# Kernel optimization log

Hardware: AMD Instinct MI355X
Metric: run time of the kernel (lower is better)

The kernel has to match this reference:

```python
import jax, jax.numpy as jnp
import numpy as np

B, S, H = 2, 256, 512
EPS = 1e-12  # TPLinker conditional LayerNorm default epsilon
NEG = -1e30  # finite stand-in for -inf in running max


def _cond_layer_norm(x, cond, Wg, Wb, gamma, beta):
    # TPLinker conditional LayerNorm: gamma/beta are modulated by a linear map of cond.
    g = gamma + cond @ Wg          # (..., H)
    b = beta + cond @ Wb           # (..., H)
    xc = x - jnp.mean(x, axis=-1, keepdims=True)
    inv = jax.lax.rsqrt(jnp.mean(xc * xc, axis=-1, keepdims=True) + EPS)
    return xc * inv * g + b


def setup_inputs() -> dict:
    key = jax.random.key(0)
    ks = jax.random.split(key, 6)
    return {
        "seq_hiddens": jax.random.normal(ks[0], (B, S, H), jnp.float32),
        "mask": jnp.ones((B, S), jnp.float32),
        "lamtha": jax.random.uniform(ks[1], (H,), jnp.float32),
        "Wg1": jax.random.normal(ks[2], (H, H), jnp.float32) * 0.02,
        "Wb1": jax.random.normal(ks[3], (H, H), jnp.float32) * 0.02,
        "g1": jnp.ones((H,), jnp.float32),
        "b1": jnp.zeros((H,), jnp.float32),
        "Wg2": jax.random.normal(ks[4], (H, H), jnp.float32) * 0.02,
        "Wb2": jax.random.normal(ks[5], (H, H), jnp.float32) * 0.02,
        "g2": jnp.ones((H,), jnp.float32),
        "b2": jnp.zeros((H,), jnp.float32),
    }


def reference(seq_hiddens, mask, lamtha, Wg1, Wb1, g1, b1, Wg2, Wb2, g2, b2):
    # mask additive penalty, broadcast over hidden (matches (1-mask)*-1000 expand)
    seq = seq_hiddens + ((1.0 - mask) * -1000.0)[:, :, None]  # (B,S,H)

    ii, jj = jnp.triu_indices(S)  # row-major pairs (i, j>=i), same order as the torch loop

    # window means over seq[i..j] via cumulative sums (replaces O(S^3) recomputation)
    csum = jnp.cumsum(seq, axis=1)                              # (B,S,H)
    lens = (jj - ii + 1).astype(seq.dtype)[None, :, None]
    mean_pairs = (csum[:, jj] - csum[:, ii] + seq[:, ii]) / lens  # (B,P,H)

    # window maxes over seq[i..j]: scan over j keeping running max per start i
    idx = jnp.arange(S)

    def step(state, j):
        sj = jnp.take(seq, j, axis=1)  # (B,H)
        new = jnp.where((idx <= j)[None, :, None],
                        jnp.maximum(state, sj[:, None, :]),
                        jnp.asarray(NEG, seq.dtype))
        return new, new

    _, Mall = jax.lax.scan(step, jnp.full((B, S, H), NEG, seq.dtype), idx)  # (S_j,B,S_i,H)
    max_pairs = Mall[jj, :, ii].transpose(1, 0, 2)  # (B,P,H)

    # mix pooling
    inner = lamtha * mean_pairs + (1.0 - lamtha) * max_pairs  # (B,P,H)

    visible = seq[:, jj]  # (B,P,H) token j
    repeat = seq[:, ii]   # (B,P,H) token i

    shaking = _cond_layer_norm(visible, repeat, Wg1, Wb1, g1, b1)
    return _cond_layer_norm(shaking, inner, Wg2, Wb2, g2, b2)
```

## Files before the change

kernel.cpp:

```cpp
#include <hip/hip_runtime.h>
#include <hip/hip_bf16.h>

typedef __hip_bfloat16 bf16;
typedef short short8 __attribute__((ext_vector_type(8)));
typedef float floatx4 __attribute__((ext_vector_type(4)));

#define S 256
#define H 512
#define P 32896
#define NROWS 65792
#define NEGF -1e30f
#define EPSF 1e-12f

#define OFF_SEQ    0u
#define OFF_CSUM   1048576u
#define OFF_LN1    2129920u
#define OFF_G1     3178496u
#define OFF_B1     4227072u
#define OFF_WCAT   5275648u
#define OFF_II     6324224u
#define OFF_JJ     6390016u
#define OFF_MU2    6455808u
#define OFF_INV2   6718976u
#define OFF_INNER  6982144u

__device__ __forceinline__ void gld_lds16(const void* g, void* l) {
    __builtin_amdgcn_global_load_lds(
        (const __attribute__((address_space(1))) void*)g,
        (__attribute__((address_space(3))) void*)l, 16, 0, 0);
}

__global__ __launch_bounds__(512) void prep_kernel(const float* __restrict__ Wg2,
                                                   const float* __restrict__ Wb2,
                                                   bf16* __restrict__ wcatT,
                                                   unsigned short* __restrict__ ii,
                                                   unsigned short* __restrict__ jj) {
    if (blockIdx.x < 1024) {
        int n = blockIdx.x, k = threadIdx.x;
        int tt = n >> 7, c = n & 127;
        int h = tt * 64 + (c & 63);
        float v = (c < 64) ? Wg2[(size_t)k * H + h] : Wb2[(size_t)k * H + h];
        wcatT[(size_t)n * H + k] = __float2bfloat16(v);
    } else {
        int p = (blockIdx.x - 1024) * 512 + threadIdx.x;
        if (p >= P) return;
        float disc = 513.0f * 513.0f - 8.0f * (float)p;
        int i = (int)((513.0f - sqrtf(disc)) * 0.5f);
        i = i < 0 ? 0 : (i > S - 1 ? S - 1 : i);
        while (i > 0 && (i * S - i * (i - 1) / 2) > p) --i;
        while (i < S - 1 && ((i + 1) * S - (i + 1) * i / 2) <= p) ++i;
        int off = i * S - i * (i - 1) / 2;
        ii[p] = (unsigned short)i;
        jj[p] = (unsigned short)(i + (p - off));
    }
}

__global__ __launch_bounds__(512) void seq_scan1_ln1(const float* __restrict__ x,
                                                     const float* __restrict__ mask,
                                                     float* __restrict__ seq, float* __restrict__ tot,
                                                     float* __restrict__ ln1) {
    __shared__ float part[8][8][2];
    __shared__ float rstat[8][2];
    int b = blockIdx.x >> 5, sc = blockIdx.x & 31, h = threadIdx.x;
    int wave = h >> 6, lane = h & 63;
    int s0 = sc * 8;
    float v[8];
    float run = 0.0f;
#pragma unroll
    for (int t = 0; t < 8; ++t) {
        int s = s0 + t;
        v[t] = x[(size_t)(b * S + s) * H + h] + (1.0f - mask[b * S + s]) * (-1000.0f);
        seq[(size_t)(b * S + s) * H + h] = v[t];
        run += v[t];
    }
    tot[(size_t)blockIdx.x * H + h] = run;
#pragma unroll
    for (int t = 0; t < 8; ++t) {
        float s = v[t], q = v[t] * v[t];
        for (int o = 1; o < 64; o <<= 1) { s += __shfl_xor(s, o); q += __shfl_xor(q, o); }
        if (lane == 0) { part[wave][t][0] = s; part[wave][t][1] = q; }
    }
    __syncthreads();
    if (h < 16) {
        int row = h >> 1, st = h & 1;
        float a = 0.0f;
#pragma unroll
        for (int w = 0; w < 8; ++w) a += part[w][row][st];
        rstat[row][st] = a;
    }
    __syncthreads();
#pragma unroll
    for (int t = 0; t < 8; ++t) {
        float m = rstat[t][0] * (1.0f / 512.0f);
        float var = rstat[t][1] * (1.0f / 512.0f) - m * m;
        var = var < 0.0f ? 0.0f : var;
        float inv = rsqrtf(var + EPSF);
        ln1[(size_t)(b * S + s0 + t) * H + h] = (v[t] - m) * inv;
    }
}

__global__ __launch_bounds__(512) void seq_scan2(const float* __restrict__ seq,
                                                 const float* __restrict__ tot,
                                                 float* __restrict__ csum) {
    int b = blockIdx.x >> 5, sc = blockIdx.x & 31, h = threadIdx.x;
    float run = 0.0f;
    for (int c = 0; c < sc; ++c) run += tot[(size_t)(b * 32 + c) * H + h];
    int s0 = sc * 8;
#pragma unroll
    for (int t = 0; t < 8; ++t) {
        run += seq[(size_t)(b * S + s0 + t) * H + h];
        csum[(size_t)(b * S + s0 + t) * H + h] = run;
    }
}

__global__ __launch_bounds__(512) void g1b1_kernel(
    const float* __restrict__ seq, const float* __restrict__ Wg1, const float* __restrict__ Wb1,
    const float* __restrict__ g1, const float* __restrict__ b1,
    float* __restrict__ G1, float* __restrict__ B1) {
    __shared__ float rowbuf[4][H];
    int grp = blockIdx.x;
    int mat = blockIdx.y;
    int h = threadIdx.x;
    int r0 = grp * 4;
    for (int r = 0; r < 4; ++r) rowbuf[r][h] = seq[(size_t)(r0 + r) * H + h];
    __syncthreads();
    const float* W = mat ? Wb1 : Wg1;
    float acc[4] = {0, 0, 0, 0};
#pragma unroll 8
    for (int k = 0; k < H; ++k) {
        float w = W[(size_t)k * H + h];
#pragma unroll
        for (int r = 0; r < 4; ++r) acc[r] += rowbuf[r][k] * w;
    }
    float bias = (mat ? b1 : g1)[h];
    float* dst = mat ? B1 : G1;
    for (int r = 0; r < 4; ++r) dst[(size_t)(r0 + r) * H + h] = acc[r] + bias;
}

__global__ __launch_bounds__(256) void inner_kernel(
    const float* __restrict__ seq, const float* __restrict__ csum,
    const float* __restrict__ lamtha, bf16* __restrict__ inner) {
    int id = blockIdx.x;
    int t = id & 255, b = id >> 8;
    int i = b ? (255 - t) : t;
    int h2 = threadIdx.x;
    float2 lam = ((const float2*)lamtha)[h2];
    float2 oml = {1.0f - lam.x, 1.0f - lam.y};
    const float2* seqb = (const float2*)(seq + (size_t)b * S * H);
    const float2* csb = (const float2*)(csum + (size_t)b * S * H);
    float2 s_i = seqb[i * 256 + h2];
    float2 c_i = csb[i * 256 + h2];
    float2 mrun = {NEGF, NEGF};
    size_t base = (size_t)b * P + (size_t)(i * S - i * (i - 1) / 2);
    __hip_bfloat162* dst = (__hip_bfloat162*)inner;
    int j = i;
#define INNER_STEP(vv, cc, jx)                                             \
    {                                                                      \
        mrun.x = fmaxf(mrun.x, vv.x);                                      \
        mrun.y = fmaxf(mrun.y, vv.y);                                      \
        float rl = 1.0f / (float)((jx) - i + 1);                           \
        float mx = (cc.x - c_i.x + s_i.x) * rl;                            \
        float my = (cc.y - c_i.y + s_i.y) * rl;                            \
        __hip_bfloat162 o;                                                 \
        o.x = __float2bfloat16(lam.x * mx + oml.x * mrun.x);               \
        o.y = __float2bfloat16(lam.y * my + oml.y * mrun.y);               \
        dst[(base + (size_t)((jx) - i)) * 256 + h2] = o;                   \
    }
    for (; j + 4 <= S; j += 4) {
        float2 v0 = seqb[(j + 0) * 256 + h2], c0 = csb[(j + 0) * 256 + h2];
        float2 v1 = seqb[(j + 1) * 256 + h2], c1 = csb[(j + 1) * 256 + h2];
        float2 v2 = seqb[(j + 2) * 256 + h2], c2 = csb[(j + 2) * 256 + h2];
        float2 v3 = seqb[(j + 3) * 256 + h2], c3 = csb[(j + 3) * 256 + h2];
        INNER_STEP(v0, c0, j + 0)
        INNER_STEP(v1, c1, j + 1)
        INNER_STEP(v2, c2, j + 2)
        INNER_STEP(v3, c3, j + 3)
    }
    for (; j < S; ++j) {
        float2 v = seqb[j * 256 + h2];
        float2 c = csb[j * 256 + h2];
        INNER_STEP(v, c, j)
    }
#undef INNER_STEP
}

__global__ void stats_kernel(const float* __restrict__ ln1, const float* __restrict__ G1,
                             const float* __restrict__ B1,
                             const unsigned short* __restrict__ ii,
                             const unsigned short* __restrict__ jj,
                             float* __restrict__ mu2, float* __restrict__ inv2) {
    int r = blockIdx.x * 4 + (threadIdx.x >> 6);
    int lane = threadIdx.x & 63;
    int b = (r >= P) ? 1 : 0;
    int p = r - b * P;
    int i = ii[p], j = jj[p];
    const float4* lp = (const float4*)(ln1 + (size_t)(b * S + j) * H);
    const float4* gp = (const float4*)(G1 + (size_t)(b * S + i) * H);
    const float4* bp = (const float4*)(B1 + (size_t)(b * S + i) * H);
    float sum = 0.0f, ss = 0.0f;
#pragma unroll
    for (int t = 0; t < 2; ++t) {
        int idx = t * 64 + lane;
        float4 a = lp[idx], g = gp[idx], bb = bp[idx];
        float v0 = a.x * g.x + bb.x, v1 = a.y * g.y + bb.y;
        float v2 = a.z * g.z + bb.z, v3 = a.w * g.w + bb.w;
        sum += (v0 + v1) + (v2 + v3);
        ss += (v0 * v0 + v1 * v1) + (v2 * v2 + v3 * v3);
    }
    for (int o = 1; o < 64; o <<= 1) { sum += __shfl_xor(sum, o); ss += __shfl_xor(ss, o); }
    if (lane == 0) {
        float m = sum * (1.0f / 512.0f);
        float var = ss * (1.0f / 512.0f) - m * m;
        var = var < 0.0f ? 0.0f : var;
        mu2[r] = m;
        inv2[r] = rsqrtf(var + EPSF);
    }
}

__global__ __launch_bounds__(256, 2) void gemm_kernel(
    const bf16* __restrict__ inner, const bf16* __restrict__ wcatT,
    const float* __restrict__ g2, const float* __restrict__ b2,
    const float* __restrict__ ln1, const float* __restrict__ G1, const float* __restrict__ B1,
    const unsigned short* __restrict__ ii, const unsigned short* __restrict__ jj,
    const float* __restrict__ mu2, const float* __restrict__ inv2,
    float* __restrict__ out) {
    extern __shared__ __align__(16) char smem[];

    const int tid = threadIdx.x;
    const int wave = tid >> 6, lane = tid & 63;
    const int q = lane >> 4, l15 = lane & 15;
    const int wm = wave & 1, wn = wave >> 1;

    const int id = blockIdx.x;
    int rb, t;
    if (id < 4096) { rb = (id >> 6) * 8 + (id & 7); t = (id >> 3) & 7; }
    else           { int w = id - 4096; rb = 512 + (w & 1); t = w >> 1; }
    const int R0 = rb * 128;

    const int srow = tid >> 3;
    const int sx8 = ((tid & 7) ^ (srow & 7)) * 8;
    const bf16* const Ag = inner + (size_t)(R0 + srow) * H + sx8;
    const bf16* const Bg = wcatT + (size_t)(t * 128 + srow) * H + sx8;

    char* const A0 = smem;
    char* const B0 = smem + 16384;
    char* const A1 = smem + 32768;
    char* const B1s = smem + 49152;

    floatx4 acc[4][4];
#pragma unroll
    for (int a = 0; a < 4; ++a)
#pragma unroll
        for (int c = 0; c < 4; ++c) acc[a][c] = (floatx4){0.f, 0.f, 0.f, 0.f};

    auto STAGE = [&](int kt, char* Ad, char* Bd) {
#pragma unroll
        for (int i2 = 0; i2 < 4; ++i2)
            gld_lds16(Ag + (size_t)i2 * 32 * H + kt * 64, Ad + i2 * 4096 + wave * 1024);
#pragma unroll
        for (int i2 = 0; i2 < 4; ++i2)
            gld_lds16(Bg + (size_t)i2 * 32 * H + kt * 64, Bd + i2 * 4096 + wave * 1024);
    };

    STAGE(0, A0, B0);
    STAGE(1, A1, B1s);
    asm volatile("s_waitcnt vmcnt(8)" ::: "memory");
    asm volatile("s_barrier" ::: "memory");

#pragma unroll
    for (int kt = 0; kt < 8; ++kt) {
        char* const As = (kt & 1) ? A1 : A0;
        char* const Bs = (kt & 1) ? B1s : B0;

        short8 bfr[4][2], af[4][2];
#pragma unroll
        for (int ks = 0; ks < 2; ++ks) {
#pragma unroll
            for (int fn = 0; fn < 4; ++fn) {
                int nr = (fn < 2 ? wn * 32 + fn * 16 : 64 + wn * 32 + (fn - 2) * 16) + l15;
                bfr[fn][ks] = *(const short8*)(Bs + nr * 128 + (((ks * 4 + q) ^ (l15 & 7)) << 4));
            }
#pragma unroll
            for (int fm = 0; fm < 4; ++fm) {
                int mr = wm * 64 + fm * 16 + l15;
                af[fm][ks] = *(const short8*)(As + mr * 128 + (((ks * 4 + q) ^ (l15 & 7)) << 4));
            }
        }

        __builtin_amdgcn_s_setprio(1);
#pragma unroll
        for (int fm = 0; fm < 4; ++fm)
#pragma unroll
            for (int fn = 0; fn < 4; ++fn)
                acc[fm][fn] = __builtin_amdgcn_mfma_f32_16x16x32_bf16(af[fm][0], bfr[fn][0], acc[fm][fn], 0, 0, 0);
        __builtin_amdgcn_s_setprio(0);

        if (kt < 6) {
            asm volatile("s_waitcnt lgkmcnt(0)" ::: "memory");
            asm volatile("s_barrier" ::: "memory");
            STAGE(kt + 2, As, Bs);
        }

        __builtin_amdgcn_s_setprio(1);
#pragma unroll
        for (int fm = 0; fm < 4; ++fm)
#pragma unroll
            for (int fn = 0; fn < 4; ++fn)
                acc[fm][fn] = __builtin_amdgcn_mfma_f32_16x16x32_bf16(af[fm][1], bfr[fn][1], acc[fm][fn], 0, 0, 0);
        __builtin_amdgcn_s_setprio(0);

        if (kt < 6) {
            asm volatile("s_waitcnt vmcnt(8)" ::: "memory");
            asm volatile("s_barrier" ::: "memory");
        } else if (kt == 6) {
            asm volatile("s_waitcnt vmcnt(0)" ::: "memory");
            asm volatile("s_barrier" ::: "memory");
        }
    }

    float g2v[2], b2v[2];
#pragma unroll
    for (int fg = 0; fg < 2; ++fg) {
        int h = t * 64 + wn * 32 + fg * 16 + l15;
        g2v[fg] = g2[h];
        b2v[fg] = b2[h];
    }
#pragma unroll
    for (int fm = 0; fm < 4; ++fm) {
#pragma unroll
        for (int r = 0; r < 4; ++r) {
            int m = wm * 64 + fm * 16 + q * 4 + r;
            int rg = R0 + m;
            int b = (rg >= P) ? 1 : 0;
            int p = rg - b * P;
            int i = ii[p], j = jj[p];
            float mu = mu2[rg], iv = inv2[rg];
            const float* lp = ln1 + (size_t)(b * S + j) * H + t * 64 + wn * 32;
            const float* gp = G1 + (size_t)(b * S + i) * H + t * 64 + wn * 32;
            const float* bp = B1 + (size_t)(b * S + i) * H + t * 64 + wn * 32;
            float* op = out + (size_t)rg * H + t * 64 + wn * 32;
#pragma unroll
            for (int fg = 0; fg < 2; ++fg) {
                int c = fg * 16 + l15;
                float s = (lp[c] * gp[c] + bp[c] - mu) * iv;
                float G2v = acc[fm][fg][r] + g2v[fg];
                float B2v = acc[fm][fg + 2][r] + b2v[fg];
                op[c] = s * G2v + B2v;
            }
        }
    }
}

extern "C" void kernel_launch(void* const* d_in, const int* in_sizes, int n_in,
                              void* d_out, int out_size, void* d_ws, size_t ws_size,
                              hipStream_t stream) {
    const float* x = (const float*)d_in[0];
    const float* mask = (const float*)d_in[1];
    const float* lamtha = (const float*)d_in[2];
    const float* Wg1 = (const float*)d_in[3];
    const float* Wb1 = (const float*)d_in[4];
    const float* g1 = (const float*)d_in[5];
    const float* b1 = (const float*)d_in[6];
    const float* Wg2 = (const float*)d_in[7];
    const float* Wb2 = (const float*)d_in[8];
    const float* g2 = (const float*)d_in[9];
    const float* b2 = (const float*)d_in[10];
    float* out = (float*)d_out;

    char* ws = (char*)d_ws;
    float* seq = (float*)(ws + OFF_SEQ);
    float* csum = (float*)(ws + OFF_CSUM);
    float* ln1 = (float*)(ws + OFF_LN1);
    float* G1 = (float*)(ws + OFF_G1);
    float* B1 = (float*)(ws + OFF_B1);
    bf16* wcatT = (bf16*)(ws + OFF_WCAT);
    unsigned short* iiA = (unsigned short*)(ws + OFF_II);
    unsigned short* jjA = (unsigned short*)(ws + OFF_JJ);
    float* mu2 = (float*)(ws + OFF_MU2);
    float* inv2 = (float*)(ws + OFF_INV2);
    bf16* inner = (bf16*)(ws + OFF_INNER);
    float* tot = (float*)(ws + OFF_INNER);

    static bool attr_set = false;
    if (!attr_set) {
        hipFuncSetAttribute((const void*)gemm_kernel,
                            hipFuncAttributeMaxDynamicSharedMemorySize, 65536);
        attr_set = true;
    }

    hipLaunchKernelGGL(prep_kernel, dim3(1089), dim3(512), 0, stream, Wg2, Wb2, wcatT, iiA, jjA);
    hipLaunchKernelGGL(seq_scan1_ln1, dim3(64), dim3(512), 0, stream, x, mask, seq, tot, ln1);
    hipLaunchKernelGGL(seq_scan2, dim3(64), dim3(512), 0, stream, seq, tot, csum);
    hipLaunchKernelGGL(g1b1_kernel, dim3(128, 2), dim3(512), 0, stream, seq, Wg1, Wb1, g1, b1, G1, B1);
    hipLaunchKernelGGL(inner_kernel, dim3(512), dim3(256), 0, stream, seq, csum, lamtha, inner);
    hipLaunchKernelGGL(stats_kernel, dim3(16448), dim3(256), 0, stream, ln1, G1, B1, iiA, jjA, mu2, inv2);
    hipLaunchKernelGGL(gemm_kernel, dim3(4112), dim3(256), 65536, stream,
                       inner, wcatT, g2, b2, ln1, G1, B1, iiA, jjA, mu2, inv2, out);
}
```

Before: 313.4 us.

## Replace cumsum pass with running sums and merge prep kernels

Drops the two-pass cumulative sum over the sequence: inner_kernel now keeps a running window sum per start index alongside the running max, so the csum buffer and the seq_scan2 kernel go away. The weight-transpose/index prep and the mask/LN1 kernel are merged into one launch, which cuts the kernel count and removes a dependency stage. g1b1 is restructured to 256 threads that each compute two output columns, with float4 reads from shared memory. These are small pre-stages relative to the large GEMM, so any saving is limited to a few microseconds of launch and memory traffic.

```diff
diff --git a/kernel.cpp b/kernel.cpp
--- a/kernel.cpp
+++ b/kernel.cpp
@@ -13,7 +13,6 @@
 #define EPSF 1e-12f
 
 #define OFF_SEQ    0u
-#define OFF_CSUM   1048576u
 #define OFF_LN1    2129920u
 #define OFF_G1     3178496u
 #define OFF_B1     4227072u
@@ -30,116 +29,121 @@
         (__attribute__((address_space(3))) void*)l, 16, 0, 0);
 }
 
-__global__ __launch_bounds__(512) void prep_kernel(const float* __restrict__ Wg2,
-                                                   const float* __restrict__ Wb2,
-                                                   bf16* __restrict__ wcatT,
-                                                   unsigned short* __restrict__ ii,
-                                                   unsigned short* __restrict__ jj) {
-    if (blockIdx.x < 1024) {
-        int n = blockIdx.x, k = threadIdx.x;
-        int tt = n >> 7, c = n & 127;
-        int h = tt * 64 + (c & 63);
-        float v = (c < 64) ? Wg2[(size_t)k * H + h] : Wb2[(size_t)k * H + h];
-        wcatT[(size_t)n * H + k] = __float2bfloat16(v);
-    } else {
-        int p = (blockIdx.x - 1024) * 512 + threadIdx.x;
-        if (p >= P) return;
-        float disc = 513.0f * 513.0f - 8.0f * (float)p;
-        int i = (int)((513.0f - sqrtf(disc)) * 0.5f);
-        i = i < 0 ? 0 : (i > S - 1 ? S - 1 : i);
-        while (i > 0 && (i * S - i * (i - 1) / 2) > p) --i;
-        while (i < S - 1 && ((i + 1) * S - (i + 1) * i / 2) <= p) ++i;
-        int off = i * S - i * (i - 1) / 2;
-        ii[p] = (unsigned short)i;
-        jj[p] = (unsigned short)(i + (p - off));
-    }
-}
-
-__global__ __launch_bounds__(512) void seq_scan1_ln1(const float* __restrict__ x,
-                                                     const float* __restrict__ mask,
-                                                     float* __restrict__ seq, float* __restrict__ tot,
-                                                     float* __restrict__ ln1) {
+__global__ __launch_bounds__(512) void fusedA_kernel(
+    const float* __restrict__ x, const float* __restrict__ mask,
+    float* __restrict__ seq, float* __restrict__ ln1,
+    const float* __restrict__ Wg2, const float* __restrict__ Wb2,
+    bf16* __restrict__ wcatT,
+    unsigned short* __restrict__ ii, unsigned short* __restrict__ jj) {
     __shared__ float part[8][8][2];
     __shared__ float rstat[8][2];
-    int b = blockIdx.x >> 5, sc = blockIdx.x & 31, h = threadIdx.x;
-    int wave = h >> 6, lane = h & 63;
-    int s0 = sc * 8;
-    float v[8];
-    float run = 0.0f;
-#pragma unroll
-    for (int t = 0; t < 8; ++t) {
-        int s = s0 + t;
-        v[t] = x[(size_t)(b * S + s) * H + h] + (1.0f - mask[b * S + s]) * (-1000.0f);
-        seq[(size_t)(b * S + s) * H + h] = v[t];
-        run += v[t];
-    }
-    tot[(size_t)blockIdx.x * H + h] = run;
-#pragma unroll
-    for (int t = 0; t < 8; ++t) {
-        float s = v[t], q = v[t] * v[t];
-        for (int o = 1; o < 64; o <<= 1) { s += __shfl_xor(s, o); q += __shfl_xor(q, o); }
-        if (lane == 0) { part[wave][t][0] = s; part[wave][t][1] = q; }
-    }
-    __syncthreads();
-    if (h < 16) {
-        int row = h >> 1, st = h & 1;
-        float a = 0.0f;
-#pragma unroll
-        for (int w = 0; w < 8; ++w) a += part[w][row][st];
-        rstat[row][st] = a;
-    }
-    __syncthreads();
-#pragma unroll
-    for (int t = 0; t < 8; ++t) {
-        float m = rstat[t][0] * (1.0f / 512.0f);
-        float var = rstat[t][1] * (1.0f / 512.0f) - m * m;
-        var = var < 0.0f ? 0.0f : var;
-        float inv = rsqrtf(var + EPSF);
-        ln1[(size_t)(b * S + s0 + t) * H + h] = (v[t] - m) * inv;
-    }
-}
-
-__global__ __launch_bounds__(512) void seq_scan2(const float* __restrict__ seq,
-                                                 const float* __restrict__ tot,
-                                                 float* __restrict__ csum) {
-    int b = blockIdx.x >> 5, sc = blockIdx.x & 31, h = threadIdx.x;
-    float run = 0.0f;
-    for (int c = 0; c < sc; ++c) run += tot[(size_t)(b * 32 + c) * H + h];
-    int s0 = sc * 8;
-#pragma unroll
-    for (int t = 0; t < 8; ++t) {
-        run += seq[(size_t)(b * S + s0 + t) * H + h];
-        csum[(size_t)(b * S + s0 + t) * H + h] = run;
-    }
-}
-
-__global__ __launch_bounds__(512) void g1b1_kernel(
+    if (blockIdx.x < 64) {
+        int b = blockIdx.x >> 5, sc = blockIdx.x & 31, h = threadIdx.x;
+        int wave = h >> 6, lane = h & 63;
+        int s0 = sc * 8;
+        float v[8];
+#pragma unroll
+        for (int t = 0; t < 8; ++t) {
+            int s = s0 + t;
+            v[t] = x[(size_t)(b * S + s) * H + h] + (1.0f - mask[b * S + s]) * (-1000.0f);
+            seq[(size_t)(b * S + s) * H + h] = v[t];
+        }
+#pragma unroll
+        for (int t = 0; t < 8; ++t) {
+            float s = v[t], q = v[t] * v[t];
+            for (int o = 1; o < 64; o <<= 1) { s += __shfl_xor(s, o); q += __shfl_xor(q, o); }
+            if (lane == 0) { part[wave][t][0] = s; part[wave][t][1] = q; }
+        }
+        __syncthreads();
+        if (h < 16) {
+            int row = h >> 1, st = h & 1;
+            float a = 0.0f;
+#pragma unroll
+            for (int w = 0; w < 8; ++w) a += part[w][row][st];
+            rstat[row][st] = a;
+        }
+        __syncthreads();
+#pragma unroll
+        for (int t = 0; t < 8; ++t) {
+            float m = rstat[t][0] * (1.0f / 512.0f);
+            float var = rstat[t][1] * (1.0f / 512.0f) - m * m;
+            var = var < 0.0f ? 0.0f : var;
+            float inv = rsqrtf(var + EPSF);
+            ln1[(size_t)(b * S + s0 + t) * H + h] = (v[t] - m) * inv;
+        }
+    } else {
+        int n = blockIdx.x - 64;
+        if (n < 1024) {
+            int k = threadIdx.x;
+            int tt = n >> 7, c = n & 127;
+            int h = tt * 64 + (c & 63);
+            float v = (c < 64) ? Wg2[(size_t)k * H + h] : Wb2[(size_t)k * H + h];
+            wcatT[(size_t)n * H + k] = __float2bfloat16(v);
+        } else {
+            int p = (n - 1024) * 512 + threadIdx.x;
+            if (p >= P) return;
+            float disc = 513.0f * 513.0f - 8.0f * (float)p;
+            int i = (int)((513.0f - sqrtf(disc)) * 0.5f);
+            i = i < 0 ? 0 : (i > S - 1 ? S - 1 : i);
+            while (i > 0 && (i * S - i * (i - 1) / 2) > p) --i;
+            while (i < S - 1 && ((i + 1) * S - (i + 1) * i / 2) <= p) ++i;
+            int off = i * S - i * (i - 1) / 2;
+            ii[p] = (unsigned short)i;
+            jj[p] = (unsigned short)(i + (p - off));
+        }
+    }
+}
+
+__global__ __launch_bounds__(256) void g1b1_kernel(
     const float* __restrict__ seq, const float* __restrict__ Wg1, const float* __restrict__ Wb1,
     const float* __restrict__ g1, const float* __restrict__ b1,
     float* __restrict__ G1, float* __restrict__ B1) {
     __shared__ float rowbuf[4][H];
     int grp = blockIdx.x;
     int mat = blockIdx.y;
-    int h = threadIdx.x;
+    int tid = threadIdx.x;
+    int h0 = tid, h1 = tid + 256;
     int r0 = grp * 4;
-    for (int r = 0; r < 4; ++r) rowbuf[r][h] = seq[(size_t)(r0 + r) * H + h];
+#pragma unroll
+    for (int r = 0; r < 4; ++r) {
+        rowbuf[r][h0] = seq[(size_t)(r0 + r) * H + h0];
+        rowbuf[r][h1] = seq[(size_t)(r0 + r) * H + h1];
+    }
     __syncthreads();
     const float* W = mat ? Wb1 : Wg1;
-    float acc[4] = {0, 0, 0, 0};
-#pragma unroll 8
-    for (int k = 0; k < H; ++k) {
-        float w = W[(size_t)k * H + h];
-#pragma unroll
-        for (int r = 0; r < 4; ++r) acc[r] += rowbuf[r][k] * w;
-    }
-    float bias = (mat ? b1 : g1)[h];
+    float acc[4][2] = {{0, 0}, {0, 0}, {0, 0}, {0, 0}};
+#pragma unroll 2
+    for (int k4 = 0; k4 < 128; ++k4) {
+        float4 a0 = ((const float4*)rowbuf[0])[k4];
+        float4 a1 = ((const float4*)rowbuf[1])[k4];
+        float4 a2 = ((const float4*)rowbuf[2])[k4];
+        float4 a3 = ((const float4*)rowbuf[3])[k4];
+        float w00 = W[(size_t)(k4 * 4 + 0) * H + h0], w01 = W[(size_t)(k4 * 4 + 0) * H + h1];
+        float w10 = W[(size_t)(k4 * 4 + 1) * H + h0], w11 = W[(size_t)(k4 * 4 + 1) * H + h1];
+        float w20 = W[(size_t)(k4 * 4 + 2) * H + h0], w21 = W[(size_t)(k4 * 4 + 2) * H + h1];
+        float w30 = W[(size_t)(k4 * 4 + 3) * H + h0], w31 = W[(size_t)(k4 * 4 + 3) * H + h1];
+        acc[0][0] += a0.x * w00 + a0.y * w10 + a0.z * w20 + a0.w * w30;
+        acc[0][1] += a0.x * w01 + a0.y * w11 + a0.z * w21 + a0.w * w31;
+        acc[1][0] += a1.x * w00 + a1.y * w10 + a1.z * w20 + a1.w * w30;
+        acc[1][1] += a1.x * w01 + a1.y * w11 + a1.z * w21 + a1.w * w31;
+        acc[2][0] += a2.x * w00 + a2.y * w10 + a2.z * w20 + a2.w * w30;
+        acc[2][1] += a2.x * w01 + a2.y * w11 + a2.z * w21 + a2.w * w31;
+        acc[3][0] += a3.x * w00 + a3.y * w10 + a3.z * w20 + a3.w * w30;
+        acc[3][1] += a3.x * w01 + a3.y * w11 + a3.z * w21 + a3.w * w31;
+    }
+    float bias0 = (mat ? b1 : g1)[h0];
+    float bias1 = (mat ? b1 : g1)[h1];
     float* dst = mat ? B1 : G1;
-    for (int r = 0; r < 4; ++r) dst[(size_t)(r0 + r) * H + h] = acc[r] + bias;
+#pragma unroll
+    for (int r = 0; r < 4; ++r) {
+        dst[(size_t)(r0 + r) * H + h0] = acc[r][0] + bias0;
+        dst[(size_t)(r0 + r) * H + h1] = acc[r][1] + bias1;
+    }
 }
 
 __global__ __launch_bounds__(256) void inner_kernel(
-    const float* __restrict__ seq, const float* __restrict__ csum,
-    const float* __restrict__ lamtha, bf16* __restrict__ inner) {
+    const float* __restrict__ seq, const float* __restrict__ lamtha,
+    bf16* __restrict__ inner) {
     int id = blockIdx.x;
     int t = id & 255, b = id >> 8;
     int i = b ? (255 - t) : t;
@@ -147,39 +151,38 @@
     float2 lam = ((const float2*)lamtha)[h2];
     float2 oml = {1.0f - lam.x, 1.0f - lam.y};
     const float2* seqb = (const float2*)(seq + (size_t)b * S * H);
-    const float2* csb = (const float2*)(csum + (size_t)b * S * H);
-    float2 s_i = seqb[i * 256 + h2];
-    float2 c_i = csb[i * 256 + h2];
     float2 mrun = {NEGF, NEGF};
+    float2 srun = {0.0f, 0.0f};
     size_t base = (size_t)b * P + (size_t)(i * S - i * (i - 1) / 2);
     __hip_bfloat162* dst = (__hip_bfloat162*)inner;
     int j = i;
-#define INNER_STEP(vv, cc, jx)                                             \
+#define INNER_STEP(vv, jx)                                                 \
     {                                                                      \
+        srun.x += vv.x;                                                    \
+        srun.y += vv.y;                                                    \
         mrun.x = fmaxf(mrun.x, vv.x);                                      \
         mrun.y = fmaxf(mrun.y, vv.y);                                      \
         float rl = 1.0f / (float)((jx) - i + 1);                           \
-        float mx = (cc.x - c_i.x + s_i.x) * rl;                            \
-        float my = (cc.y - c_i.y + s_i.y) * rl;                            \
+        float mx = srun.x * rl;                                            \
+        float my = srun.y * rl;                                            \
         __hip_bfloat162 o;                                                 \
         o.x = __float2bfloat16(lam.x * mx + oml.x * mrun.x);               \
         o.y = __float2bfloat16(lam.y * my + oml.y * mrun.y);               \
         dst[(base + (size_t)((jx) - i)) * 256 + h2] = o;                   \
     }
     for (; j + 4 <= S; j += 4) {
-        float2 v0 = seqb[(j + 0) * 256 + h2], c0 = csb[(j + 0) * 256 + h2];
-        float2 v1 = seqb[(j + 1) * 256 + h2], c1 = csb[(j + 1) * 256 + h2];
-        float2 v2 = seqb[(j + 2) * 256 + h2], c2 = csb[(j + 2) * 256 + h2];
-        float2 v3 = seqb[(j + 3) * 256 + h2], c3 = csb[(j + 3) * 256 + h2];
-        INNER_STEP(v0, c0, j + 0)
-        INNER_STEP(v1, c1, j + 1)
-        INNER_STEP(v2, c2, j + 2)
-        INNER_STEP(v3, c3, j + 3)
+        float2 v0 = seqb[(j + 0) * 256 + h2];
+        float2 v1 = seqb[(j + 1) * 256 + h2];
+        float2 v2 = seqb[(j + 2) * 256 + h2];
+        float2 v3 = seqb[(j + 3) * 256 + h2];
+        INNER_STEP(v0, j + 0)
+        INNER_STEP(v1, j + 1)
+        INNER_STEP(v2, j + 2)
+        INNER_STEP(v3, j + 3)
     }
     for (; j < S; ++j) {
         float2 v = seqb[j * 256 + h2];
-        float2 c = csb[j * 256 + h2];
-        INNER_STEP(v, c, j)
+        INNER_STEP(v, j)
     }
 #undef INNER_STEP
 }
@@ -369,7 +372,6 @@
 
     char* ws = (char*)d_ws;
     float* seq = (float*)(ws + OFF_SEQ);
-    float* csum = (float*)(ws + OFF_CSUM);
     float* ln1 = (float*)(ws + OFF_LN1);
     float* G1 = (float*)(ws + OFF_G1);
     float* B1 = (float*)(ws + OFF_B1);
@@ -379,7 +381,6 @@
     float* mu2 = (float*)(ws + OFF_MU2);
     float* inv2 = (float*)(ws + OFF_INV2);
     bf16* inner = (bf16*)(ws + OFF_INNER);
-    float* tot = (float*)(ws + OFF_INNER);
 
     static bool attr_set = false;
     if (!attr_set) {
@@ -388,12 +389,14 @@
         attr_set = true;
     }
 
-    hipLaunchKernelGGL(prep_kernel, dim3(1089), dim3(512), 0, stream, Wg2, Wb2, wcatT, iiA, jjA);
-    hipLaunchKernelGGL(seq_scan1_ln1, dim3(64), dim3(512), 0, stream, x, mask, seq, tot, ln1);
-    hipLaunchKernelGGL(seq_scan2, dim3(64), dim3(512), 0, stream, seq, tot, csum);
-    hipLaunchKernelGGL(g1b1_kernel, dim3(128, 2), dim3(512), 0, stream, seq, Wg1, Wb1, g1, b1, G1, B1);
-    hipLaunchKernelGGL(inner_kernel, dim3(512), dim3(256), 0, stream, seq, csum, lamtha, inner);
-    hipLaunchKernelGGL(stats_kernel, dim3(16448), dim3(256), 0, stream, ln1, G1, B1, iiA, jjA, mu2, inv2);
+    hipLaunchKernelGGL(fusedA_kernel, dim3(1153), dim3(512), 0, stream,
+                       x, mask, seq, ln1, Wg2, Wb2, wcatT, iiA, jjA);
+    hipLaunchKernelGGL(g1b1_kernel, dim3(128, 2), dim3(256), 0, stream,
+                       seq, Wg1, Wb1, g1, b1, G1, B1);
+    hipLaunchKernelGGL(inner_kernel, dim3(512), dim3(256), 0, stream,
+                       seq, lamtha, inner);
+    hipLaunchKernelGGL(stats_kernel, dim3(16448), dim3(256), 0, stream,
+                       ln1, G1, B1, iiA, jjA, mu2, inv2);
     hipLaunchKernelGGL(gemm_kernel, dim3(4112), dim3(256), 65536, stream,
                        inner, wcatT, g2, b2, ln1, G1, B1, iiA, jjA, mu2, inv2, out);
 }
```

Result: faster. 301.8 us (-3.7%).
